# Kernel optimization log

Hardware: AMD Instinct MI355X
Metric: run time of the kernel (lower is better)

The kernel has to match this reference:

```python
import math
import jax, jax.numpy as jnp
import numpy as np

B, T, E, H = 2, 2048, 1024, 16
HS = E // H  # head size = 64
NEG = jnp.float32(-1e10)


def setup_inputs() -> dict:
    key = jax.random.key(0)
    ks = jax.random.split(key, 7)
    return {
        "query": jax.random.normal(ks[0], (B, T, E), jnp.float32),
        "key": jax.random.normal(ks[1], (B, T, E), jnp.float32),
        "value": jax.random.normal(ks[2], (B, T, E), jnp.float32),
        "Wq": jax.random.normal(ks[3], (E, E), jnp.float32) * 0.02,
        "Wk": jax.random.normal(ks[4], (E, E), jnp.float32) * 0.02,
        "Wv": jax.random.normal(ks[5], (E, E), jnp.float32) * 0.02,
        "Wp": jax.random.normal(ks[6], (E, E), jnp.float32) * 0.02,
    }


def reference(query, key, value, Wq, Wk, Wv, Wp):
    # QKV projections (no bias), split into heads: [B, H, T, HS]
    q = (query @ Wq).reshape(B, T, H, HS).transpose(0, 2, 1, 3)
    k = (key @ Wk).reshape(B, T, H, HS).transpose(0, 2, 1, 3)
    v = (value @ Wv).reshape(B, T, H, HS).transpose(0, 2, 1, 3)
    # scaled dot-product scores [B, H, T, T]
    att = jnp.einsum("bhqd,bhkd->bhqk", q, k) / math.sqrt(HS)
    # additive causal mask (tril allowed)
    causal = jnp.tril(jnp.ones((T, T), dtype=att.dtype))
    att = att + jnp.where(causal == 0, NEG, jnp.float32(0.0))[None, None]
    att = jax.nn.softmax(att, axis=-1)
    # dropout rate 0 / deterministic -> identity
    y = jnp.einsum("bhqk,bhkd->bhqd", att, v)
    y = y.transpose(0, 2, 1, 3).reshape(B, T, E)
    y = y @ Wp
    return y
```

## Files before the change

kernel.cpp:

```cpp
#include <hip/hip_runtime.h>

#define TB 2
#define TT 2048
#define TE 1024
#define TH 16
#define THS 64
#define TM (TB * TT)

typedef __attribute__((ext_vector_type(8))) short short8;
typedef __attribute__((ext_vector_type(4))) float f32x4;

__device__ __forceinline__ f32x4 mfma16(short8 a, short8 b, f32x4 c) {
    return __builtin_amdgcn_mfma_f32_16x16x32_bf16(a, b, c, 0, 0, 0);
}

__device__ __forceinline__ void gload_lds16(const void* g, void* l) {
    __builtin_amdgcn_global_load_lds(
        (const __attribute__((address_space(1))) void*)g,
        (__attribute__((address_space(3))) void*)l, 16, 0, 0);
}

__device__ __forceinline__ unsigned short f2bf(float f) {
    unsigned int u = __float_as_uint(f);
    u += 0x7fff + ((u >> 16) & 1);
    return (unsigned short)(u >> 16);
}

__device__ __forceinline__ unsigned cvtpk_bf16(float lo, float hi) {
    unsigned r;
    asm("v_cvt_pk_bf16_f32 %0, %1, %2" : "=v"(r) : "v"(lo), "v"(hi));
    return r;
}

__global__ __launch_bounds__(256) void cast3_f32_bf16(
    const float* __restrict__ a, const float* __restrict__ b,
    const float* __restrict__ c, unsigned short* __restrict__ oa,
    unsigned short* __restrict__ ob, unsigned short* __restrict__ oc, int n4) {
    const float* src = (blockIdx.y == 0) ? a : (blockIdx.y == 1) ? b : c;
    unsigned short* dst = (blockIdx.y == 0) ? oa : (blockIdx.y == 1) ? ob : oc;
    int i = blockIdx.x * 256 + threadIdx.x;
    if (i < n4) {
        float4 v = ((const float4*)src)[i];
        ushort4 o;
        o.x = f2bf(v.x); o.y = f2bf(v.y); o.z = f2bf(v.z); o.w = f2bf(v.w);
        ((ushort4*)dst)[i] = o;
    }
}

__global__ __launch_bounds__(256) void transpose_cast_w4(
    const float* __restrict__ W0, const float* __restrict__ W1,
    const float* __restrict__ W2, const float* __restrict__ W3,
    unsigned short* __restrict__ T0, unsigned short* __restrict__ T1,
    unsigned short* __restrict__ T2, unsigned short* __restrict__ T3) {
    __shared__ float Ts[32][33];
    const int z = blockIdx.z;
    const float* W = (z == 0) ? W0 : (z == 1) ? W1 : (z == 2) ? W2 : W3;
    unsigned short* Wt = (z == 0) ? T0 : (z == 1) ? T1 : (z == 2) ? T2 : T3;
    const int r0 = blockIdx.y * 32, c0 = blockIdx.x * 32;
    const int t = threadIdx.x;
    const int r = t >> 3, c = (t & 7) * 4;
    float4 v = *(const float4*)&W[(size_t)(r0 + r) * TE + c0 + c];
    Ts[r][c] = v.x; Ts[r][c + 1] = v.y; Ts[r][c + 2] = v.z; Ts[r][c + 3] = v.w;
    __syncthreads();
    ushort4 o;
    o.x = f2bf(Ts[c + 0][r]); o.y = f2bf(Ts[c + 1][r]);
    o.z = f2bf(Ts[c + 2][r]); o.w = f2bf(Ts[c + 3][r]);
    *(ushort4*)&Wt[(size_t)(c0 + r) * TE + r0 + c] = o;
}

__global__ __launch_bounds__(512, 2) void gemm_qkv(
    const unsigned short* __restrict__ qc, const unsigned short* __restrict__ kc,
    const unsigned short* __restrict__ vc, const unsigned short* __restrict__ Wqt,
    const unsigned short* __restrict__ Wkt, const unsigned short* __restrict__ Wvt,
    unsigned short* __restrict__ Qb, unsigned short* __restrict__ Kb,
    unsigned short* __restrict__ Vt) {
    __shared__ unsigned short LDS[65536];

    const int z = blockIdx.z;
    const unsigned short* A  = (z == 0) ? qc : (z == 1) ? kc : vc;
    const unsigned short* Bt = (z == 0) ? Wqt : (z == 1) ? Wkt : Wvt;

    const int tid = threadIdx.x;
    const int wv = tid >> 6, lane = tid & 63;
    const int wr = wv >> 2, wc = wv & 3;
    const int quad = lane >> 4, l16 = lane & 15;
    const int bm = blockIdx.x * 256, bn = blockIdx.y * 256;

    const int srow = lane >> 2;
    const int scol = (((lane & 3) ^ ((srow >> 1) & 3))) * 8;
    const int rchunk = (quad ^ ((l16 >> 1) & 3)) * 8;

    f32x4 acc[8][4];
    const f32x4 fz = {0.f, 0.f, 0.f, 0.f};
    #pragma unroll
    for (int i = 0; i < 8; ++i)
        #pragma unroll
        for (int j = 0; j < 4; ++j) acc[i][j] = fz;

    auto stageA = [&](int t, int hi) {
        const int buf = t & 1, k0 = t * 64;
        unsigned short* base = &LDS[buf * 16384];
        #pragma unroll
        for (int j = 0; j < 2; ++j) {
            const int e = wv * 2 + j;
            const int kk = e >> 3, i3 = e & 7;
            const int cr = hi * 4 + (i3 & 3) + ((i3 >> 2) << 3);
            gload_lds16(A + (size_t)(bm + cr * 16 + srow) * TE + k0 + kk * 32 + scol,
                        base + kk * 8192 + cr * 512 + lane * 8);
        }
    };
    auto stageB = [&](int t, int hi) {
        const int buf = t & 1, k0 = t * 64;
        unsigned short* base = &LDS[32768 + buf * 16384];
        #pragma unroll
        for (int j = 0; j < 2; ++j) {
            const int e = wv * 2 + j;
            const int kk = e >> 3, i3 = e & 7;
            const int cc = ((i3 >> 1) << 2) + (i3 & 1) + hi * 2;
            gload_lds16(Bt + (size_t)(bn + cc * 16 + srow) * TE + k0 + kk * 32 + scol,
                        base + kk * 8192 + cc * 512 + lane * 8);
        }
    };

    auto ktile = [&](int t, int buf, bool st, bool predrain) {
        const unsigned short* Al = &LDS[buf * 16384];
        const unsigned short* Bl = &LDS[32768 + buf * 16384];
        short8 af[4][2], blo[2][2], bhi[2][2];
        #pragma unroll
        for (int mi = 0; mi < 4; ++mi)
            #pragma unroll
            for (int kk = 0; kk < 2; ++kk)
                af[mi][kk] = *(const short8*)&Al[kk * 8192 + (wr * 8 + mi) * 512 + l16 * 32 + rchunk];
        #pragma unroll
        for (int nj = 0; nj < 2; ++nj)
            #pragma unroll
            for (int kk = 0; kk < 2; ++kk)
                blo[nj][kk] = *(const short8*)&Bl[kk * 8192 + (wc * 4 + nj) * 512 + l16 * 32 + rchunk];
        __builtin_amdgcn_s_barrier();
        asm volatile("s_waitcnt lgkmcnt(0)" ::: "memory");
        __builtin_amdgcn_sched_barrier(0);
        __builtin_amdgcn_s_setprio(1);
        #pragma unroll
        for (int mi = 0; mi < 4; ++mi)
            #pragma unroll
            for (int nj = 0; nj < 2; ++nj)
                #pragma unroll
                for (int kk = 0; kk < 2; ++kk)
                    acc[mi][nj] = mfma16(af[mi][kk], blo[nj][kk], acc[mi][nj]);
        __builtin_amdgcn_s_setprio(0);
        __builtin_amdgcn_sched_barrier(0);
        __builtin_amdgcn_s_barrier();
        #pragma unroll
        for (int nj = 0; nj < 2; ++nj)
            #pragma unroll
            for (int kk = 0; kk < 2; ++kk)
                bhi[nj][kk] = *(const short8*)&Bl[kk * 8192 + (wc * 4 + 2 + nj) * 512 + l16 * 32 + rchunk];
        if (st) stageA(t + 2, 0);
        __builtin_amdgcn_s_barrier();
        asm volatile("s_waitcnt lgkmcnt(0)" ::: "memory");
        __builtin_amdgcn_sched_barrier(0);
        __builtin_amdgcn_s_setprio(1);
        #pragma unroll
        for (int mi = 0; mi < 4; ++mi)
            #pragma unroll
            for (int nj = 0; nj < 2; ++nj)
                #pragma unroll
                for (int kk = 0; kk < 2; ++kk)
                    acc[mi][2 + nj] = mfma16(af[mi][kk], bhi[nj][kk], acc[mi][2 + nj]);
        __builtin_amdgcn_s_setprio(0);
        __builtin_amdgcn_sched_barrier(0);
        __builtin_amdgcn_s_barrier();
        #pragma unroll
        for (int mi = 0; mi < 4; ++mi)
            #pragma unroll
            for (int kk = 0; kk < 2; ++kk)
                af[mi][kk] = *(const short8*)&Al[kk * 8192 + (wr * 8 + 4 + mi) * 512 + l16 * 32 + rchunk];
        if (st) stageB(t + 2, 0);
        __builtin_amdgcn_s_barrier();
        asm volatile("s_waitcnt lgkmcnt(0)" ::: "memory");
        __builtin_amdgcn_sched_barrier(0);
        __builtin_amdgcn_s_setprio(1);
        #pragma unroll
        for (int mi = 0; mi < 4; ++mi)
            #pragma unroll
            for (int nj = 0; nj < 2; ++nj)
                #pragma unroll
                for (int kk = 0; kk < 2; ++kk)
                    acc[4 + mi][nj] = mfma16(af[mi][kk], blo[nj][kk], acc[4 + mi][nj]);
        __builtin_amdgcn_s_setprio(0);
        __builtin_amdgcn_sched_barrier(0);
        __builtin_amdgcn_s_barrier();
        if (st) { stageB(t + 2, 1); stageA(t + 2, 1); }
        __builtin_amdgcn_s_barrier();
        __builtin_amdgcn_s_setprio(1);
        #pragma unroll
        for (int mi = 0; mi < 4; ++mi)
            #pragma unroll
            for (int nj = 0; nj < 2; ++nj)
                #pragma unroll
                for (int kk = 0; kk < 2; ++kk)
                    acc[4 + mi][2 + nj] = mfma16(af[mi][kk], bhi[nj][kk], acc[4 + mi][2 + nj]);
        __builtin_amdgcn_s_setprio(0);
        __builtin_amdgcn_sched_barrier(0);
        if (st) {
            asm volatile("s_waitcnt vmcnt(8)" ::: "memory");
        } else if (predrain) {
            asm volatile("s_waitcnt vmcnt(0)" ::: "memory");
        }
        __builtin_amdgcn_s_barrier();
    };

    stageA(0, 0); stageB(0, 0); stageB(0, 1); stageA(0, 1);
    stageA(1, 0); stageB(1, 0); stageB(1, 1); stageA(1, 1);
    asm volatile("s_waitcnt vmcnt(8)" ::: "memory");
    __builtin_amdgcn_s_barrier();

    #pragma unroll 1
    for (int t = 0; t < 14; t += 2) {
        ktile(t, 0, true, false);
        ktile(t + 1, 1, true, false);
    }
    ktile(14, 0, false, true);
    ktile(15, 1, false, false);

    if (z < 2) {
        unsigned short* Cb = (z == 0) ? Qb : Kb;
        const float sc = (z == 0) ? 0.18033688011112042f : 1.0f;
        #pragma unroll
        for (int mi = 0; mi < 8; ++mi)
            #pragma unroll
            for (int nj = 0; nj < 4; ++nj) {
                const int m0 = bm + wr * 128 + mi * 16 + quad * 4;
                const int n = bn + wc * 64 + nj * 16 + l16;
                #pragma unroll
                for (int r = 0; r < 4; ++r)
                    Cb[(size_t)(m0 + r) * TE + n] = f2bf(acc[mi][nj][r] * sc);
            }
    } else {
        #pragma unroll
        for (int mi = 0; mi < 8; ++mi)
            #pragma unroll
            for (int nj = 0; nj < 4; ++nj) {
                const int m0 = bm + wr * 128 + mi * 16 + quad * 4;
                const int n = bn + wc * 64 + nj * 16 + l16;
                ushort4 o;
                o.x = f2bf(acc[mi][nj][0]); o.y = f2bf(acc[mi][nj][1]);
                o.z = f2bf(acc[mi][nj][2]); o.w = f2bf(acc[mi][nj][3]);
                size_t idx = ((size_t)((m0 >> 11) * TH + (n >> 6)) * THS + (n & 63)) * TT + (m0 & (TT - 1));
                *(ushort4*)&Vt[idx] = o;
            }
    }
}

__global__ __launch_bounds__(256, 2) void gemm_out(
    const unsigned short* __restrict__ A, const unsigned short* __restrict__ Bt,
    float* __restrict__ C) {
    __shared__ unsigned short As[2][128 * 32];
    __shared__ unsigned short Bs[2][64 * 32];

    const int tid = threadIdx.x;
    const int w = tid >> 6, lane = tid & 63;
    const int quad = lane >> 4, l16 = lane & 15;
    const int bm = blockIdx.x * 128, bn = blockIdx.y * 64;
    const int wm = (w >> 1) * 64, wn = (w & 1) * 32;

    f32x4 acc[4][2];
    const f32x4 fz = {0.f, 0.f, 0.f, 0.f};
    #pragma unroll
    for (int i = 0; i < 4; ++i)
        #pragma unroll
        for (int j = 0; j < 2; ++j) acc[i][j] = fz;

    const int srow = lane >> 2;
    const int scol = (((lane & 3) ^ ((srow >> 1) & 3))) * 8;
    const int rchunk = (quad ^ ((l16 >> 1) & 3)) * 8;

    auto stage = [&](int k0, int buf) {
        #pragma unroll
        for (int i = 0; i < 3; ++i) {
            const int ch = w * 3 + i;
            if (ch < 8)
                gload_lds16(A + (size_t)(bm + ch * 16 + srow) * TE + k0 + scol,
                            &As[buf][ch * 512 + lane * 8]);
            else
                gload_lds16(Bt + (size_t)(bn + (ch - 8) * 16 + srow) * TE + k0 + scol,
                            &Bs[buf][(ch - 8) * 512 + lane * 8]);
        }
    };

    stage(0, 0);
    int cur = 0;
    for (int k0 = 0; k0 < TE; k0 += 32) {
        __syncthreads();
        if (k0 + 32 < TE) stage(k0 + 32, cur ^ 1);

        short8 af[4], bf[2];
        #pragma unroll
        for (int i = 0; i < 4; ++i)
            af[i] = *(const short8*)&As[cur][(wm + i * 16 + l16) * 32 + rchunk];
        #pragma unroll
        for (int j = 0; j < 2; ++j)
            bf[j] = *(const short8*)&Bs[cur][(wn + j * 16 + l16) * 32 + rchunk];
        #pragma unroll
        for (int i = 0; i < 4; ++i)
            #pragma unroll
            for (int j = 0; j < 2; ++j)
                acc[i][j] = mfma16(af[i], bf[j], acc[i][j]);
        cur ^= 1;
    }

    #pragma unroll
    for (int i = 0; i < 4; ++i)
        #pragma unroll
        for (int j = 0; j < 2; ++j) {
            const int m0 = bm + wm + i * 16 + quad * 4;
            const int n = bn + wn + j * 16 + l16;
            #pragma unroll
            for (int r = 0; r < 4; ++r)
                C[(size_t)(m0 + r) * TE + n] = acc[i][j][r];
        }
}

__global__ __launch_bounds__(512, 4) void attn_mfma(
    const unsigned short* __restrict__ Q, const unsigned short* __restrict__ K,
    const unsigned short* __restrict__ Vt, unsigned short* __restrict__ O) {
    __shared__ unsigned short S[2][16384];
    __shared__ float L0[64];

    const int tid = threadIdx.x;
    const int lane = tid & 63;
    const int wv = tid >> 6;
    const int wk = wv >> 2;
    const int wl = wv & 3;
    const int quad = lane >> 4, l16 = lane & 15;

    const int lin = blockIdx.x;
    const int bh = (lin & 7) * 4 + ((lin >> 3) & 3);
    const int p = lin >> 5;
    const int b = bh >> 4, h = bh & 15;
    const int itA = (TT / 64) - 1 - p;
    const int itB = p;

    const unsigned short* Kg = K + (size_t)b * TT * TE + h * THS;
    const unsigned short* Vg = Vt + (size_t)bh * THS * TT;

    const size_t qrA = (size_t)(b * TT + itA * 64 + wl * 16 + l16) * TE + h * THS;
    const size_t qrB = (size_t)(b * TT + itB * 64 + wl * 16 + l16) * TE + h * THS;
    const short8 aqA0 = *(const short8*)&Q[qrA + quad * 8];
    const short8 aqA1 = *(const short8*)&Q[qrA + 32 + quad * 8];
    const short8 aqB0 = *(const short8*)&Q[qrB + quad * 8];
    const short8 aqB1 = *(const short8*)&Q[qrB + 32 + quad * 8];

    const f32x4 fz = {0.f, 0.f, 0.f, 0.f};
    const int srow = lane >> 2;
    const int scol = (((lane & 3) ^ ((srow >> 1) & 3))) * 8;
    const int rchunk = (quad ^ ((l16 >> 1) & 3)) * 8;

    unsigned short* Sw = S[wk];
    float* Sf = (float*)S;

    auto stageKV = [&](int jt, int it, int buf) {
        const int k0 = (jt > it ? it : jt) * 64;
        if (wl < 2) {
            #pragma unroll
            for (int j = 0; j < 4; ++j) {
                const int ee = wl * 4 + j;
                const int kk = ee >> 2, r16 = (ee & 3) * 16;
                gload_lds16(Kg + (size_t)(k0 + r16 + srow) * TE + kk * 32 + scol,
                            &Sw[buf * 4096 + ee * 512 + lane * 8]);
            }
        } else {
            #pragma unroll
            for (int j = 0; j < 4; ++j) {
                const int ee = (wl - 2) * 4 + j;
                const int kk = ee >> 2, r16 = (ee & 3) * 16;
                gload_lds16(Vg + (size_t)(r16 + srow) * TT + k0 + kk * 32 + scol,
                            &Sw[8192 + buf * 4096 + ee * 512 + lane * 8]);
            }
        }
    };

    int cur = 0;
    const int src0 = ((quad & 1) << 5) + l16;
    const bool hi = quad >= 2;

    auto segment = [&](int it, short8 aq0, short8 aq1, int nextit ) {
        const int h0 = (it + 2) >> 1;
        const int base = wk ? h0 : 0;
        f32x4 acc_o[4];
        #pragma unroll
        for (int ni = 0; ni < 4; ++ni) acc_o[ni] = fz;
        float lacc = 0.f;
        const int q0 = it * 64;
        const int qg = q0 + wl * 16 + l16;

        for (int i = 0; i < h0; ++i) {
            const int jt = base + i;
            __syncthreads();
            if (i + 1 < h0) stageKV(base + i + 1, it, cur ^ 1);
            else if (nextit >= 0) stageKV(wk ? ((nextit + 2) >> 1) : 0, nextit, cur ^ 1);

            f32x4 s[4];
            #pragma unroll
            for (int ni = 0; ni < 4; ++ni) {
                short8 kf0 = *(const short8*)&Sw[cur * 4096 + (ni * 16 + l16) * 32 + rchunk];
                short8 kf1 = *(const short8*)&Sw[cur * 4096 + 2048 + (ni * 16 + l16) * 32 + rchunk];
                s[ni] = mfma16(kf0, aq0, fz);
                s[ni] = mfma16(kf1, aq1, s[ni]);
            }

            const int k0 = jt * 64;
            float pv[4][4];
            if (jt < it) {
                #pragma unroll
                for (int ni = 0; ni < 4; ++ni)
                    #pragma unroll
                    for (int r = 0; r < 4; ++r) {
                        pv[ni][r] = __builtin_amdgcn_exp2f(s[ni][r]);
                        lacc += pv[ni][r];
                    }
            } else if (jt == it) {
                #pragma unroll
                for (int ni = 0; ni < 4; ++ni) {
                    const int kpb = k0 + ni * 16 + quad * 4;
                    #pragma unroll
                    for (int r = 0; r < 4; ++r) {
                        float e = __builtin_amdgcn_exp2f(s[ni][r]);
                        pv[ni][r] = (kpb + r > qg) ? 0.f : e;
                        lacc += pv[ni][r];
                    }
                }
            } else {
                #pragma unroll
                for (int ni = 0; ni < 4; ++ni)
                    #pragma unroll
                    for (int r = 0; r < 4; ++r) pv[ni][r] = 0.f;
            }

            unsigned int pd0[4], pd1[4];
            #pragma unroll
            for (int t = 0; t < 4; ++t) {
                pd0[t] = cvtpk_bf16(pv[t][0], pv[t][1]);
                pd1[t] = cvtpk_bf16(pv[t][2], pv[t][3]);
            }

            short8 pf[2];
            #pragma unroll
            for (int c = 0; c < 2; ++c) {
                const int tl = 2 * c, th = 2 * c + 1;
                unsigned d0l = __shfl(pd0[tl], src0),      d0h = __shfl(pd0[th], src0);
                unsigned d1l = __shfl(pd1[tl], src0),      d1h = __shfl(pd1[th], src0);
                unsigned d2l = __shfl(pd0[tl], src0 + 16), d2h = __shfl(pd0[th], src0 + 16);
                unsigned d3l = __shfl(pd1[tl], src0 + 16), d3h = __shfl(pd1[th], src0 + 16);
                union { unsigned u[4]; short8 s8; } pk;
                pk.u[0] = hi ? d0h : d0l;
                pk.u[1] = hi ? d1h : d1l;
                pk.u[2] = hi ? d2h : d2l;
                pk.u[3] = hi ? d3h : d3l;
                pf[c] = pk.s8;
            }

            #pragma unroll
            for (int ni = 0; ni < 4; ++ni) {
                short8 v0 = *(const short8*)&Sw[8192 + cur * 4096 + (ni * 16 + l16) * 32 + rchunk];
                short8 v1 = *(const short8*)&Sw[8192 + cur * 4096 + 2048 + (ni * 16 + l16) * 32 + rchunk];
                acc_o[ni] = mfma16(pf[0], v0, acc_o[ni]);
                acc_o[ni] = mfma16(pf[1], v1, acc_o[ni]);
            }
            cur ^= 1;
        }

        lacc += __shfl_xor(lacc, 16);
        lacc += __shfl_xor(lacc, 32);

        __syncthreads();
        const int fb = cur ^ 1;
        if (wk == 0) {
            #pragma unroll
            for (int ni = 0; ni < 4; ++ni)
                #pragma unroll
                for (int r = 0; r < 4; ++r) {
                    const int row = wl * 16 + quad * 4 + r;
                    const int idx = row * 64 + ni * 16 + l16;
                    Sf[(idx >> 11) * 8192 + fb * 2048 + (idx & 2047)] = acc_o[ni][r];
                }
            if (quad == 0) L0[wl * 16 + l16] = lacc;
        }
        __syncthreads();
        if (wk == 1) {
            const float lf = lacc + L0[wl * 16 + l16];
            float linv[4];
            #pragma unroll
            for (int r = 0; r < 4; ++r)
                linv[r] = 1.0f / __shfl(lf, quad * 4 + r);
            unsigned short* Og = O + (size_t)(b * TT + q0 + wl * 16 + quad * 4) * TE + h * THS;
            #pragma unroll
            for (int r = 0; r < 4; ++r)
                #pragma unroll
                for (int ni = 0; ni < 4; ++ni) {
                    const int row = wl * 16 + quad * 4 + r;
                    const int idx = row * 64 + ni * 16 + l16;
                    const float o = acc_o[ni][r] + Sf[(idx >> 11) * 8192 + fb * 2048 + (idx & 2047)];
                    Og[(size_t)r * TE + ni * 16 + l16] = f2bf(o * linv[r]);
                }
        }
    };

    stageKV(wk ? ((itA + 2) >> 1) : 0, itA, 0);
    segment(itA, aqA0, aqA1, itB);
    segment(itB, aqB0, aqB1, -1);
}

extern "C" void kernel_launch(void* const* d_in, const int* in_sizes, int n_in,
                              void* d_out, int out_size, void* d_ws, size_t ws_size,
                              hipStream_t stream) {
    const float* q  = (const float*)d_in[0];
    const float* k  = (const float*)d_in[1];
    const float* v  = (const float*)d_in[2];
    const float* Wq = (const float*)d_in[3];
    const float* Wk = (const float*)d_in[4];
    const float* Wv = (const float*)d_in[5];
    const float* Wp = (const float*)d_in[6];
    float* out = (float*)d_out;

    const size_t se = (size_t)TM * TE;
    unsigned short* qc  = (unsigned short*)d_ws;
    unsigned short* kc  = qc + se;
    unsigned short* vc  = kc + se;
    unsigned short* Qb  = vc + se;
    unsigned short* Kb  = Qb + se;
    unsigned short* Vt  = Kb + se;
    unsigned short* Ob  = Vt + se;
    unsigned short* Wqt = Ob + se;
    unsigned short* Wkt = Wqt + (size_t)TE * TE;
    unsigned short* Wvt = Wkt + (size_t)TE * TE;
    unsigned short* Wpt = Wvt + (size_t)TE * TE;

    const int n4 = (int)(se / 4);
    cast3_f32_bf16<<<dim3(n4 / 256, 3), 256, 0, stream>>>(q, k, v, qc, kc, vc, n4);
    transpose_cast_w4<<<dim3(TE / 32, TE / 32, 4), 256, 0, stream>>>(
        Wq, Wk, Wv, Wp, Wqt, Wkt, Wvt, Wpt);

    gemm_qkv<<<dim3(TM / 256, TE / 256, 3), 512, 0, stream>>>(
        qc, kc, vc, Wqt, Wkt, Wvt, Qb, Kb, Vt);

    attn_mfma<<<512, 512, 0, stream>>>(Qb, Kb, Vt, Ob);

    gemm_out<<<dim3(TM / 128, TE / 64), 256, 0, stream>>>(Ob, Wpt, out);
}
```

Baseline: 206.5 us.

## Rework causal attention to 128-row query tiles with 32x32 MFMA and triple buffering

```diff
diff --git a/kernel.cpp b/kernel.cpp
--- a/kernel.cpp
+++ b/kernel.cpp
@@ -9,9 +9,13 @@
 
 typedef __attribute__((ext_vector_type(8))) short short8;
 typedef __attribute__((ext_vector_type(4))) float f32x4;
+typedef __attribute__((ext_vector_type(16))) float f32x16;
 
 __device__ __forceinline__ f32x4 mfma16(short8 a, short8 b, f32x4 c) {
     return __builtin_amdgcn_mfma_f32_16x16x32_bf16(a, b, c, 0, 0, 0);
+}
+__device__ __forceinline__ f32x16 mfma32(short8 a, short8 b, f32x16 c) {
+    return __builtin_amdgcn_mfma_f32_32x32x16_bf16(a, b, c, 0, 0, 0);
 }
 
 __device__ __forceinline__ void gload_lds16(const void* g, void* l) {
@@ -30,6 +34,9 @@
     unsigned r;
     asm("v_cvt_pk_bf16_f32 %0, %1, %2" : "=v"(r) : "v"(lo), "v"(hi));
     return r;
+}
+__device__ __forceinline__ void plswap(unsigned& a, unsigned& b) {
+    asm("v_permlane32_swap_b32 %0, %1" : "+v"(a), "+v"(b));
 }
 
 __global__ __launch_bounds__(256) void cast3_f32_bf16(
@@ -321,53 +328,53 @@
         }
 }
 
-__global__ __launch_bounds__(512, 4) void attn_mfma(
+__global__ __launch_bounds__(512, 2) void attn_mfma(
     const unsigned short* __restrict__ Q, const unsigned short* __restrict__ K,
     const unsigned short* __restrict__ Vt, unsigned short* __restrict__ O) {
-    __shared__ unsigned short S[2][16384];
-    __shared__ float L0[64];
+    __shared__ unsigned short S[49152];
+    __shared__ float L0[128];
 
     const int tid = threadIdx.x;
     const int lane = tid & 63;
     const int wv = tid >> 6;
     const int wk = wv >> 2;
     const int wl = wv & 3;
-    const int quad = lane >> 4, l16 = lane & 15;
+    const int rl = lane & 31, x = lane >> 5;
 
     const int lin = blockIdx.x;
-    const int bh = (lin & 7) * 4 + ((lin >> 3) & 3);
+    const int bh = lin & 31;
     const int p = lin >> 5;
     const int b = bh >> 4, h = bh & 15;
-    const int itA = (TT / 64) - 1 - p;
-    const int itB = p;
+    const int itA = 15 - p, itB = p;
+    const int hA = itA + 1, hB = itB + 1;
 
     const unsigned short* Kg = K + (size_t)b * TT * TE + h * THS;
     const unsigned short* Vg = Vt + (size_t)bh * THS * TT;
 
-    const size_t qrA = (size_t)(b * TT + itA * 64 + wl * 16 + l16) * TE + h * THS;
-    const size_t qrB = (size_t)(b * TT + itB * 64 + wl * 16 + l16) * TE + h * THS;
-    const short8 aqA0 = *(const short8*)&Q[qrA + quad * 8];
-    const short8 aqA1 = *(const short8*)&Q[qrA + 32 + quad * 8];
-    const short8 aqB0 = *(const short8*)&Q[qrB + quad * 8];
-    const short8 aqB1 = *(const short8*)&Q[qrB + 32 + quad * 8];
-
-    const f32x4 fz = {0.f, 0.f, 0.f, 0.f};
+    short8 aqA[4], aqB[4];
+    {
+        const size_t rA = (size_t)(b * TT + itA * 128 + wl * 32 + rl) * TE + h * THS + x * 8;
+        const size_t rB = (size_t)(b * TT + itB * 128 + wl * 32 + rl) * TE + h * THS + x * 8;
+        #pragma unroll
+        for (int c = 0; c < 4; ++c) {
+            aqA[c] = *(const short8*)&Q[rA + c * 16];
+            aqB[c] = *(const short8*)&Q[rB + c * 16];
+        }
+    }
+
     const int srow = lane >> 2;
     const int scol = (((lane & 3) ^ ((srow >> 1) & 3))) * 8;
-    const int rchunk = (quad ^ ((l16 >> 1) & 3)) * 8;
-
-    unsigned short* Sw = S[wk];
-    float* Sf = (float*)S;
-
-    auto stageKV = [&](int jt, int it, int buf) {
-        const int k0 = (jt > it ? it : jt) * 64;
+    unsigned short* Sg = S + wk * 24576;
+
+    auto stage = [&](int jt, int buf) {
+        const int k0 = jt * 64;
         if (wl < 2) {
             #pragma unroll
             for (int j = 0; j < 4; ++j) {
                 const int ee = wl * 4 + j;
                 const int kk = ee >> 2, r16 = (ee & 3) * 16;
                 gload_lds16(Kg + (size_t)(k0 + r16 + srow) * TE + kk * 32 + scol,
-                            &Sw[buf * 4096 + ee * 512 + lane * 8]);
+                            &Sg[buf * 4096 + ee * 512 + lane * 8]);
             }
         } else {
             #pragma unroll
@@ -375,140 +382,145 @@
                 const int ee = (wl - 2) * 4 + j;
                 const int kk = ee >> 2, r16 = (ee & 3) * 16;
                 gload_lds16(Vg + (size_t)(r16 + srow) * TT + k0 + kk * 32 + scol,
-                            &Sw[8192 + buf * 4096 + ee * 512 + lane * 8]);
-            }
-        }
-    };
-
-    int cur = 0;
-    const int src0 = ((quad & 1) << 5) + l16;
-    const bool hi = quad >= 2;
-
-    auto segment = [&](int it, short8 aq0, short8 aq1, int nextit ) {
-        const int h0 = (it + 2) >> 1;
-        const int base = wk ? h0 : 0;
-        f32x4 acc_o[4];
-        #pragma unroll
-        for (int ni = 0; ni < 4; ++ni) acc_o[ni] = fz;
+                            &Sg[12288 + buf * 4096 + ee * 512 + lane * 8]);
+            }
+        }
+    };
+    auto stageS = [&](int s) {
+        if (s >= 17) return;
+        const int it = (s < hA) ? itA : itB;
+        const int loc = (s < hA) ? s : s - hA;
+        const int jt = (wk ? it + 1 : 0) + loc;
+        stage(jt, s % 3);
+    };
+
+    stageS(0); stageS(1);
+
+    const int xr = (rl >> 1) & 3;
+
+    auto run_seg = [&](int it, const short8* aq, int sBase, int hSeg) {
+        const int q0 = it * 128;
+        const int qv = q0 + wl * 32 + rl;
+        const int qwMin = q0 + wl * 32;
+        f32x16 accO0, accO1;
+        #pragma unroll
+        for (int i = 0; i < 16; ++i) { accO0[i] = 0.f; accO1[i] = 0.f; }
         float lacc = 0.f;
-        const int q0 = it * 64;
-        const int qg = q0 + wl * 16 + l16;
-
-        for (int i = 0; i < h0; ++i) {
-            const int jt = base + i;
-            __syncthreads();
-            if (i + 1 < h0) stageKV(base + i + 1, it, cur ^ 1);
-            else if (nextit >= 0) stageKV(wk ? ((nextit + 2) >> 1) : 0, nextit, cur ^ 1);
-
-            f32x4 s[4];
-            #pragma unroll
-            for (int ni = 0; ni < 4; ++ni) {
-                short8 kf0 = *(const short8*)&Sw[cur * 4096 + (ni * 16 + l16) * 32 + rchunk];
-                short8 kf1 = *(const short8*)&Sw[cur * 4096 + 2048 + (ni * 16 + l16) * 32 + rchunk];
-                s[ni] = mfma16(kf0, aq0, fz);
-                s[ni] = mfma16(kf1, aq1, s[ni]);
-            }
-
+
+        for (int i = 0; i < hSeg; ++i) {
+            const int s = sBase + i;
+            const int buf = s % 3;
+            if (s == 16) { asm volatile("s_waitcnt vmcnt(0)" ::: "memory"); }
+            else         { asm volatile("s_waitcnt vmcnt(4)" ::: "memory"); }
+            __builtin_amdgcn_s_barrier();
+            __builtin_amdgcn_sched_barrier(0);
+            stageS(s + 2);
+
+            const int jt = (wk ? it + 1 : 0) + i;
             const int k0 = jt * 64;
-            float pv[4][4];
-            if (jt < it) {
-                #pragma unroll
-                for (int ni = 0; ni < 4; ++ni)
-                    #pragma unroll
-                    for (int r = 0; r < 4; ++r) {
-                        pv[ni][r] = __builtin_amdgcn_exp2f(s[ni][r]);
-                        lacc += pv[ni][r];
+            const unsigned short* Kb = &Sg[buf * 4096];
+            const unsigned short* Vb = &Sg[12288 + buf * 4096];
+
+            f32x16 sa0, sa1;
+            #pragma unroll
+            for (int i2 = 0; i2 < 16; ++i2) { sa0[i2] = 0.f; sa1[i2] = 0.f; }
+            #pragma unroll
+            for (int c = 0; c < 4; ++c) {
+                const int off = (c >> 1) * 2048 + ((((c & 1) * 2 + x) ^ xr)) * 8;
+                short8 kf0 = *(const short8*)&Kb[off + rl * 32];
+                short8 kf1 = *(const short8*)&Kb[off + (32 + rl) * 32];
+                sa0 = mfma32(kf0, aq[c], sa0);
+                sa1 = mfma32(kf1, aq[c], sa1);
+            }
+
+            const bool open = (k0 + 63 <= qwMin);
+            short8 pb[4];
+            #pragma unroll
+            for (int mt = 0; mt < 2; ++mt) {
+                float pv[16];
+                #pragma unroll
+                for (int r = 0; r < 16; ++r) {
+                    const float sv = (mt == 0) ? sa0[r] : sa1[r];
+                    float e = __builtin_amdgcn_exp2f(sv);
+                    if (!open) {
+                        const int kg = k0 + mt * 32 + (r & 3) + 8 * (r >> 2) + 4 * x;
+                        e = (kg > qv) ? 0.f : e;
                     }
-            } else if (jt == it) {
-                #pragma unroll
-                for (int ni = 0; ni < 4; ++ni) {
-                    const int kpb = k0 + ni * 16 + quad * 4;
-                    #pragma unroll
-                    for (int r = 0; r < 4; ++r) {
-                        float e = __builtin_amdgcn_exp2f(s[ni][r]);
-                        pv[ni][r] = (kpb + r > qg) ? 0.f : e;
-                        lacc += pv[ni][r];
-                    }
+                    pv[r] = e;
+                    lacc += e;
                 }
-            } else {
-                #pragma unroll
-                for (int ni = 0; ni < 4; ++ni)
-                    #pragma unroll
-                    for (int r = 0; r < 4; ++r) pv[ni][r] = 0.f;
-            }
-
-            unsigned int pd0[4], pd1[4];
-            #pragma unroll
-            for (int t = 0; t < 4; ++t) {
-                pd0[t] = cvtpk_bf16(pv[t][0], pv[t][1]);
-                pd1[t] = cvtpk_bf16(pv[t][2], pv[t][3]);
-            }
-
-            short8 pf[2];
-            #pragma unroll
-            for (int c = 0; c < 2; ++c) {
-                const int tl = 2 * c, th = 2 * c + 1;
-                unsigned d0l = __shfl(pd0[tl], src0),      d0h = __shfl(pd0[th], src0);
-                unsigned d1l = __shfl(pd1[tl], src0),      d1h = __shfl(pd1[th], src0);
-                unsigned d2l = __shfl(pd0[tl], src0 + 16), d2h = __shfl(pd0[th], src0 + 16);
-                unsigned d3l = __shfl(pd1[tl], src0 + 16), d3h = __shfl(pd1[th], src0 + 16);
-                union { unsigned u[4]; short8 s8; } pk;
-                pk.u[0] = hi ? d0h : d0l;
-                pk.u[1] = hi ? d1h : d1l;
-                pk.u[2] = hi ? d2h : d2l;
-                pk.u[3] = hi ? d3h : d3l;
-                pf[c] = pk.s8;
-            }
-
-            #pragma unroll
-            for (int ni = 0; ni < 4; ++ni) {
-                short8 v0 = *(const short8*)&Sw[8192 + cur * 4096 + (ni * 16 + l16) * 32 + rchunk];
-                short8 v1 = *(const short8*)&Sw[8192 + cur * 4096 + 2048 + (ni * 16 + l16) * 32 + rchunk];
-                acc_o[ni] = mfma16(pf[0], v0, acc_o[ni]);
-                acc_o[ni] = mfma16(pf[1], v1, acc_o[ni]);
-            }
-            cur ^= 1;
-        }
-
-        lacc += __shfl_xor(lacc, 16);
+                unsigned w0 = cvtpk_bf16(pv[0], pv[1]),   w1 = cvtpk_bf16(pv[2], pv[3]);
+                unsigned w2 = cvtpk_bf16(pv[4], pv[5]),   w3 = cvtpk_bf16(pv[6], pv[7]);
+                unsigned w4 = cvtpk_bf16(pv[8], pv[9]),   w5 = cvtpk_bf16(pv[10], pv[11]);
+                unsigned w6 = cvtpk_bf16(pv[12], pv[13]), w7 = cvtpk_bf16(pv[14], pv[15]);
+                plswap(w0, w2); plswap(w1, w3);
+                plswap(w4, w6); plswap(w5, w7);
+                union { unsigned u[4]; short8 s8; } f0, f1;
+                f0.u[0] = w0; f0.u[1] = w1; f0.u[2] = w2; f0.u[3] = w3;
+                f1.u[0] = w4; f1.u[1] = w5; f1.u[2] = w6; f1.u[3] = w7;
+                pb[mt * 2] = f0.s8; pb[mt * 2 + 1] = f1.s8;
+            }
+
+            __builtin_amdgcn_s_setprio(1);
+            #pragma unroll
+            for (int c = 0; c < 4; ++c) {
+                const int off = (c >> 1) * 2048 + ((((c & 1) * 2 + x) ^ xr)) * 8;
+                short8 vf0 = *(const short8*)&Vb[off + rl * 32];
+                short8 vf1 = *(const short8*)&Vb[off + (32 + rl) * 32];
+                accO0 = mfma32(vf0, pb[c], accO0);
+                accO1 = mfma32(vf1, pb[c], accO1);
+            }
+            __builtin_amdgcn_s_setprio(0);
+        }
+
         lacc += __shfl_xor(lacc, 32);
 
         __syncthreads();
-        const int fb = cur ^ 1;
+        const int lastS = sBase + hSeg - 1;
+        const int fb = lastS % 3;
         if (wk == 0) {
             #pragma unroll
-            for (int ni = 0; ni < 4; ++ni)
-                #pragma unroll
-                for (int r = 0; r < 4; ++r) {
-                    const int row = wl * 16 + quad * 4 + r;
-                    const int idx = row * 64 + ni * 16 + l16;
-                    Sf[(idx >> 11) * 8192 + fb * 2048 + (idx & 2047)] = acc_o[ni][r];
+            for (int dt = 0; dt < 2; ++dt)
+                #pragma unroll
+                for (int q4 = 0; q4 < 4; ++q4) {
+                    const int i16 = ((dt ^ ((lane >> 2) & 1)) << 4) + ((q4 ^ (lane & 3)) << 2);
+                    const int flat = (wl * 64 + lane) * 32 + i16;
+                    const int chunk = flat >> 11, offf = flat & 2047;
+                    float* dst = (float*)&S[(chunk >> 1) * 24576 + (chunk & 1) * 12288 + fb * 4096] + offf;
+                    float4 vstv;
+                    if (dt == 0) { vstv.x = accO0[q4*4+0]; vstv.y = accO0[q4*4+1]; vstv.z = accO0[q4*4+2]; vstv.w = accO0[q4*4+3]; }
+                    else         { vstv.x = accO1[q4*4+0]; vstv.y = accO1[q4*4+1]; vstv.z = accO1[q4*4+2]; vstv.w = accO1[q4*4+3]; }
+                    *(float4*)dst = vstv;
                 }
-            if (quad == 0) L0[wl * 16 + l16] = lacc;
+            if (lane < 32) L0[wl * 32 + rl] = lacc;
         }
         __syncthreads();
         if (wk == 1) {
-            const float lf = lacc + L0[wl * 16 + l16];
-            float linv[4];
-            #pragma unroll
-            for (int r = 0; r < 4; ++r)
-                linv[r] = 1.0f / __shfl(lf, quad * 4 + r);
-            unsigned short* Og = O + (size_t)(b * TT + q0 + wl * 16 + quad * 4) * TE + h * THS;
-            #pragma unroll
-            for (int r = 0; r < 4; ++r)
-                #pragma unroll
-                for (int ni = 0; ni < 4; ++ni) {
-                    const int row = wl * 16 + quad * 4 + r;
-                    const int idx = row * 64 + ni * 16 + l16;
-                    const float o = acc_o[ni][r] + Sf[(idx >> 11) * 8192 + fb * 2048 + (idx & 2047)];
-                    Og[(size_t)r * TE + ni * 16 + l16] = f2bf(o * linv[r]);
+            const float lf = lacc + L0[wl * 32 + rl];
+            const float linv = 1.0f / lf;
+            unsigned short* Og = O + (size_t)(b * TT + q0 + wl * 32 + rl) * TE + h * THS;
+            #pragma unroll
+            for (int dt = 0; dt < 2; ++dt)
+                #pragma unroll
+                for (int q4 = 0; q4 < 4; ++q4) {
+                    const int i16 = ((dt ^ ((lane >> 2) & 1)) << 4) + ((q4 ^ (lane & 3)) << 2);
+                    const int flat = (wl * 64 + lane) * 32 + i16;
+                    const int chunk = flat >> 11, offf = flat & 2047;
+                    const float4 vld = *(const float4*)((const float*)&S[(chunk >> 1) * 24576 + (chunk & 1) * 12288 + fb * 4096] + offf);
+                    float o0, o1, o2, o3;
+                    if (dt == 0) { o0 = accO0[q4*4+0] + vld.x; o1 = accO0[q4*4+1] + vld.y; o2 = accO0[q4*4+2] + vld.z; o3 = accO0[q4*4+3] + vld.w; }
+                    else         { o0 = accO1[q4*4+0] + vld.x; o1 = accO1[q4*4+1] + vld.y; o2 = accO1[q4*4+2] + vld.z; o3 = accO1[q4*4+3] + vld.w; }
+                    const int dbase = 8 * q4 + 4 * x + 32 * dt;
+                    ushort4 o;
+                    o.x = f2bf(o0 * linv); o.y = f2bf(o1 * linv);
+                    o.z = f2bf(o2 * linv); o.w = f2bf(o3 * linv);
+                    *(ushort4*)&Og[dbase] = o;
                 }
         }
     };
 
-    stageKV(wk ? ((itA + 2) >> 1) : 0, itA, 0);
-    segment(itA, aqA0, aqA1, itB);
-    segment(itB, aqB0, aqB1, -1);
+    run_seg(itA, aqA, 0, hA);
+    run_seg(itB, aqB, hA, hB);
 }
 
 extern "C" void kernel_launch(void* const* d_in, const int* in_sizes, int n_in,
@@ -544,7 +556,7 @@
     gemm_qkv<<<dim3(TM / 256, TE / 256, 3), 512, 0, stream>>>(
         qc, kc, vc, Wqt, Wkt, Wvt, Qb, Kb, Vt);
 
-    attn_mfma<<<512, 512, 0, stream>>>(Qb, Kb, Vt, Ob);
+    attn_mfma<<<256, 512, 0, stream>>>(Qb, Kb, Vt, Ob);
 
     gemm_out<<<dim3(TM / 128, TE / 64), 256, 0, stream>>>(Ob, Wpt, out);
 }
```

Result: no change. 204.8 us (-0.8%).
